# Kernel tuning notes

Measured on AMD Instinct MI355X. Metric: run time of the kernel, lower is better.

## Reference

```python
import jax, jax.numpy as jnp
import numpy as np

B, S, F = 64, 512, 1024
D_MODEL, D_MEM, D_IN, H, D_OUT, N_SYNC, T, H_NLM = 2048, 32, 1024, 16, 1000, 512, 16, 32
DH = D_IN // H


def _ln(x, g, b):
    m = x.mean(-1, keepdims=True)
    v = ((x - m) ** 2).mean(-1, keepdims=True)
    return (x - m) * jax.lax.rsqrt(v + 1e-5) * g + b


def setup_inputs() -> dict:
    key = jax.random.key(0)
    ks = jax.random.split(key, 24)
    def n(i, shape, fan):
        return jax.random.normal(ks[i], shape, jnp.float32) * (fan ** -0.5)
    u = 1.0 / np.sqrt(D_MODEL)
    uh = 1.0 / np.sqrt(D_MODEL + D_MEM)
    return dict(
        x=jax.random.normal(ks[0], (B, S, F), jnp.float32),
        W_kv=n(1, (F, D_IN), F), b_kv=jnp.zeros((D_IN,)),
        g_kv=jnp.ones((D_IN,)), be_kv=jnp.zeros((D_IN,)),
        W_q=n(2, (N_SYNC, D_IN), N_SYNC), b_q=jnp.zeros((D_IN,)),
        W_aq=n(3, (D_IN, D_IN), D_IN), b_aq=jnp.zeros((D_IN,)),
        W_ak=n(4, (D_IN, D_IN), D_IN), b_ak=jnp.zeros((D_IN,)),
        W_av=n(5, (D_IN, D_IN), D_IN), b_av=jnp.zeros((D_IN,)),
        W_ao=n(6, (D_IN, D_IN), D_IN), b_ao=jnp.zeros((D_IN,)),
        W_s1=n(7, (D_IN + D_MODEL, D_MODEL), D_IN + D_MODEL), b_s1=jnp.zeros((D_MODEL,)),
        W_s2=n(8, (D_MODEL, D_MODEL), D_MODEL), b_s2=jnp.zeros((D_MODEL,)),
        g_s=jnp.ones((D_MODEL,)), be_s=jnp.zeros((D_MODEL,)),
        W_n1=n(9, (D_MODEL, D_MEM, H_NLM), D_MEM), b_n1=jnp.zeros((D_MODEL, H_NLM)),
        W_n2=n(10, (D_MODEL, H_NLM), H_NLM), b_n2=jnp.zeros((D_MODEL,)),
        g_n=jnp.ones((D_MODEL,)), be_n=jnp.zeros((D_MODEL,)),
        init_state=jax.random.uniform(ks[11], (D_MODEL,), jnp.float32, -u, u),
        init_hist=jax.random.uniform(ks[12], (D_MODEL, D_MEM), jnp.float32, -uh, uh),
        decay_action=jax.random.uniform(ks[13], (N_SYNC,), jnp.float32, 0.0, 2.0),
        decay_out=jax.random.uniform(ks[14], (N_SYNC,), jnp.float32, 0.0, 2.0),
        W_out=n(15, (N_SYNC, D_OUT), N_SYNC), b_out=jnp.zeros((D_OUT,)),
        idx_la=jax.random.randint(ks[16], (N_SYNC,), 0, D_MODEL),
        idx_ra=jax.random.randint(ks[17], (N_SYNC,), 0, D_MODEL),
        idx_lo=jax.random.randint(ks[18], (N_SYNC,), 0, D_MODEL),
        idx_ro=jax.random.randint(ks[19], (N_SYNC,), 0, D_MODEL),
    )


def reference(x, W_kv, b_kv, g_kv, be_kv, W_q, b_q, W_aq, b_aq, W_ak, b_ak,
              W_av, b_av, W_ao, b_ao, W_s1, b_s1, W_s2, b_s2, g_s, be_s,
              W_n1, b_n1, W_n2, b_n2, g_n, be_n, init_state, init_hist,
              decay_action, decay_out, W_out, b_out,
              idx_la, idx_ra, idx_lo, idx_ro):
    # kv features: Linear + LayerNorm, fixed across ticks -> project k,v once
    kv = _ln(x @ W_kv + b_kv, g_kv, be_kv)                      # (B,S,D_IN)
    kh = (kv @ W_ak + b_ak).reshape(B, S, H, DH)
    vh = (kv @ W_av + b_av).reshape(B, S, H, DH)
    # learnable exponential decay r = exp(-clamp(p,0,15))
    rA = jnp.exp(-jnp.clip(decay_action, 0.0, 15.0))[None, :]
    rO = jnp.exp(-jnp.clip(decay_out, 0.0, 15.0))[None, :]
    act0 = jnp.broadcast_to(init_state, (B, D_MODEL))
    hist0 = jnp.broadcast_to(init_hist, (B, D_MODEL, D_MEM))
    # out-sync initialized before loop (None branch): alpha=prod, beta=1
    aO0 = act0[:, idx_lo] * act0[:, idx_ro]
    bO0 = jnp.ones_like(aO0)
    # action-sync None branch at tick0 == recurrence from alpha=beta=0
    aA0 = jnp.zeros((B, N_SYNC), x.dtype)
    bA0 = jnp.zeros((B, N_SYNC), x.dtype)

    def step(carry, _):
        act, hist, aA, bA, aO, bO = carry
        pA = act[:, idx_la] * act[:, idx_ra]                    # paired-neuron gather
        aA = rA * aA + pA
        bA = rA * bA + 1.0
        sync_a = aA * jax.lax.rsqrt(bA)
        q = sync_a @ W_q + b_q                                  # (B,D_IN)
        qh = (q @ W_aq + b_aq).reshape(B, H, DH)
        attn_w = jax.nn.softmax(jnp.einsum('bhd,bshd->bhs', qh, kh) / np.sqrt(DH), axis=-1)
        attn = jnp.einsum('bhs,bshd->bhd', attn_w, vh).reshape(B, D_IN) @ W_ao + b_ao
        pre = jnp.concatenate([attn, act], axis=-1)             # (B, D_IN+D_MODEL)
        pre_act = _ln(jax.nn.gelu(pre @ W_s1 + b_s1) @ W_s2 + b_s2, g_s, be_s)
        hist = jnp.concatenate([hist[:, :, 1:], pre_act[:, :, None]], axis=-1)
        # per-neuron deep NLM over the memory window
        hmid = jax.nn.relu(jnp.einsum('bdm,dmh->bdh', hist, W_n1) + b_n1)
        act = _ln(jnp.einsum('bdh,dh->bd', hmid, W_n2) + b_n2, g_n, be_n)
        pO = act[:, idx_lo] * act[:, idx_ro]
        aO = rO * aO + pO
        bO = rO * bO + 1.0
        pred = (aO * jax.lax.rsqrt(bO)) @ W_out + b_out         # (B,D_OUT)
        logp = jax.nn.log_softmax(pred, axis=-1)
        ne = -(jnp.exp(logp) * logp).sum(-1) / np.log(D_OUT)    # normalized entropy
        return (act, hist, aA, bA, aO, bO), (pred, ne)

    _, (preds, nes) = jax.lax.scan(step, (act0, hist0, aA0, bA0, aO0, bO0), None, length=T)
    predictions = jnp.transpose(preds, (1, 2, 0))               # (B,D_OUT,T)
    certainties = jnp.transpose(jnp.stack([nes, 1.0 - nes], axis=1), (2, 1, 0))  # (B,2,T)
    return predictions, certainties
```

## Files before the change

kernel.cpp:

```cpp
#include <hip/hip_runtime.h>
#include <hip/hip_bf16.h>


#define B_ 64
#define S_ 512
#define F_ 1024
#define DMODEL 2048
#define DMEM 32
#define DIN 1024
#define NH 16
#define DH 64
#define DOUT 1000
#define NSYNC 512
#define TICKS 16
#define HNLM 32
#define HIST_W 48

typedef __attribute__((ext_vector_type(8))) short short8;
typedef __attribute__((ext_vector_type(4))) float f32x4;

__device__ inline void store_f(float* p, float v) { *p = v; }
__device__ inline void store_f(__hip_bfloat16* p, float v) { *p = __float2bfloat16(v); }

__device__ inline short f2bs(float f) {
  __hip_bfloat16 h = __float2bfloat16(f);
  return *reinterpret_cast<short*>(&h);
}

__device__ inline float bfs(short x) {
  return __uint_as_float(((unsigned)(unsigned short)x) << 16);
}

__device__ inline float gelu_f(float x) {
  float x3 = x * x * x;
  return 0.5f * x * (1.f + tanhf(0.7978845608028654f * (x + 0.044715f * x3)));
}

__device__ inline float bf_lo(unsigned v) { return __uint_as_float(v << 16); }
__device__ inline float bf_hi(unsigned v) { return __uint_as_float(v & 0xffff0000u); }

__global__ __launch_bounds__(256) void transpose_bf16_kernel(const float* __restrict__ W,
                                                             __hip_bfloat16* __restrict__ Wt,
                                                             int K, int N, int Npad, int ldw,
                                                             int koff) {
  __shared__ float t[32][33];
  const int tx = threadIdx.x, ty = threadIdx.y;
  const int n0 = blockIdx.x * 32, k0 = blockIdx.y * 32;
#pragma unroll
  for (int i = 0; i < 4; i++) {
    int k = k0 + ty + i * 8;
    t[ty + i * 8][tx] = (k < K && n0 + tx < N) ? W[(size_t)k * N + n0 + tx] : 0.f;
  }
  __syncthreads();
#pragma unroll
  for (int i = 0; i < 4; i++) {
    int n = n0 + ty + i * 8;
    if (n < Npad && k0 + tx < K)
      Wt[(size_t)n * ldw + koff + k0 + tx] = __float2bfloat16(t[tx][ty + i * 8]);
  }
}

__global__ void conv_bf16_kernel(const float* __restrict__ src, __hip_bfloat16* __restrict__ dst,
                                 int n) {
  int i = blockIdx.x * 256 + threadIdx.x;
  if (i < n) dst[i] = __float2bfloat16(src[i]);
}

__global__ void bqaq_kernel(const float* __restrict__ b_q, const float* __restrict__ b_aq,
                            const __hip_bfloat16* __restrict__ Wt_aq, float* __restrict__ b_qaq) {
  int n = blockIdx.x * 256 + threadIdx.x;
  if (n >= DIN) return;
  const __hip_bfloat16* wr = Wt_aq + (size_t)n * DIN;
  float s = b_aq[n];
  for (int k = 0; k < DIN; k++) s += b_q[k] * __bfloat162float(wr[k]);
  b_qaq[n] = s;
}

__global__ void bs1c_kernel(const float* __restrict__ b_s1, const float* __restrict__ b_ao,
                            const float* __restrict__ W_s1, float* __restrict__ b_s1c) {
  int n = blockIdx.x * 256 + threadIdx.x;
  if (n >= DMODEL) return;
  float s = b_s1[n];
  for (int k = 0; k < DIN; k++) s += b_ao[k] * W_s1[(size_t)k * DMODEL + n];
  b_s1c[n] = s;
}

__device__ inline short8 load_chunk(const __hip_bfloat16* p) {
  return *reinterpret_cast<const short8*>(p);
}
__device__ inline short8 load_chunk(const float* p) {
  short8 r;
#pragma unroll
  for (int j = 0; j < 8; j++) r[j] = f2bs(p[j]);
  return r;
}

template <int TRANSC, typename TA, typename TC>
__global__ __launch_bounds__(256) void gemm_big(const TA* __restrict__ A,
                                                const __hip_bfloat16* __restrict__ Bt,
                                                const float* __restrict__ bias,
                                                TC* __restrict__ C, int M, int N, int K) {
  __shared__ short lsA[128 * 64];
  __shared__ short lsB[128 * 64];
  const int tid = threadIdx.x;
  const int l = tid & 63, w = tid >> 6;
  const int wr = (w >> 1) * 64, wc = (w & 1) * 64;
  const int nwg = gridDim.x * gridDim.y;
  const int flat = blockIdx.y * gridDim.x + blockIdx.x;
  const int wk = (flat & 7) * (nwg >> 3) + (flat >> 3);
  const int brow = (wk / gridDim.x) * 128, bcol = (wk % gridDim.x) * 128;
  f32x4 acc[4][4];
#pragma unroll
  for (int i = 0; i < 4; i++)
#pragma unroll
    for (int j = 0; j < 4; j++)
#pragma unroll
      for (int r = 0; r < 4; r++) acc[i][j][r] = 0.f;

  short8 ra[4], rb[4];
  auto gload = [&](int k0) {
#pragma unroll
    for (int q = 0; q < 4; q++) {
      int i = tid + q * 256;
      int row = i >> 3, c = i & 7;
      ra[q] = load_chunk(A + (size_t)(brow + row) * K + k0 + c * 8);
      rb[q] = load_chunk(Bt + (size_t)(bcol + row) * K + k0 + c * 8);
    }
  };
  auto lwrite = [&]() {
#pragma unroll
    for (int q = 0; q < 4; q++) {
      int i = tid + q * 256;
      int row = i >> 3, c = i & 7;
      int sw = c ^ (row & 7);
      *reinterpret_cast<short8*>(&lsA[row * 64 + sw * 8]) = ra[q];
      *reinterpret_cast<short8*>(&lsB[row * 64 + sw * 8]) = rb[q];
    }
  };
  gload(0);
  for (int k0 = 0; k0 < K; k0 += 64) {
    __syncthreads();
    lwrite();
    if (k0 + 64 < K) gload(k0 + 64);
    __syncthreads();
#pragma unroll
    for (int ks = 0; ks < 2; ks++) {
      short8 af[4], bfv[4];
#pragma unroll
      for (int mi = 0; mi < 4; mi++) {
        int row = wr + mi * 16 + (l & 15);
        int c = ks * 4 + (l >> 4);
        af[mi] = *reinterpret_cast<const short8*>(&lsA[row * 64 + (c ^ (row & 7)) * 8]);
      }
#pragma unroll
      for (int ni = 0; ni < 4; ni++) {
        int row = wc + ni * 16 + (l & 15);
        int c = ks * 4 + (l >> 4);
        bfv[ni] = *reinterpret_cast<const short8*>(&lsB[row * 64 + (c ^ (row & 7)) * 8]);
      }
#pragma unroll
      for (int mi = 0; mi < 4; mi++)
#pragma unroll
        for (int ni = 0; ni < 4; ni++)
          acc[mi][ni] =
              __builtin_amdgcn_mfma_f32_16x16x32_bf16(af[mi], bfv[ni], acc[mi][ni], 0, 0, 0);
    }
  }
#pragma unroll
  for (int mi = 0; mi < 4; mi++)
#pragma unroll
    for (int ni = 0; ni < 4; ni++)
#pragma unroll
      for (int r = 0; r < 4; r++) {
        int row = brow + wr + mi * 16 + (l >> 4) * 4 + r;
        int col = bcol + wc + ni * 16 + (l & 15);
        float v = acc[mi][ni][r];
        if (bias) v += bias[col];
        if (TRANSC == 1) {
          store_f(&C[(size_t)col * M + row], v);
        } else if (TRANSC == 2) {
          int bb = row >> 9, s = row & 511, hh = col >> 6, dd = col & 63;
          store_f(&C[(((size_t)(bb * 16 + hh) * 512) + s) * 64 + dd], v);
        } else if (TRANSC == 3) {
          int bb = row >> 9, s = row & 511, hh2 = col >> 6, dd = col & 63;
          size_t base = (hh2 >= 16) ? (size_t)B_ * S_ * DIN : 0;
          store_f(&C[base + (((size_t)(bb * 16 + (hh2 & 15)) * 512) + s) * 64 + dd], v);
        } else {
          store_f(&C[(size_t)row * N + col], v);
        }
      }
}

template <typename TOUT>
__global__ __launch_bounds__(256) void ln_kernel(const float* __restrict__ x,
                                                 const float* __restrict__ g,
                                                 const float* __restrict__ be,
                                                 TOUT* __restrict__ out, int C,
                                                 size_t row_stride, int col_stride) {
  const int row = blockIdx.x;
  const int tid = threadIdx.x;
  const float* xr = x + (size_t)row * C;
  float s = 0.f, s2 = 0.f;
  for (int c = tid; c < C; c += 256) {
    float v = xr[c];
    s += v;
    s2 += v * v;
  }
  __shared__ float r1[256], r2[256];
  r1[tid] = s;
  r2[tid] = s2;
  __syncthreads();
  for (int st = 128; st > 0; st >>= 1) {
    if (tid < st) {
      r1[tid] += r1[tid + st];
      r2[tid] += r2[tid + st];
    }
    __syncthreads();
  }
  float mean = r1[0] / C;
  float var = r2[0] / C - mean * mean;
  float inv = 1.0f / sqrtf(var + 1e-5f);
  for (int c = tid; c < C; c += 256) {
    float v = (xr[c] - mean) * inv * g[c] + be[c];
    store_f(&out[(size_t)row * row_stride + (size_t)c * col_stride], v);
  }
}

__global__ void init_pre_kernel(const float* __restrict__ init_state,
                                __hip_bfloat16* __restrict__ pre) {
  int i = blockIdx.x * 256 + threadIdx.x;
  if (i >= B_ * DMODEL) return;
  int b = i >> 11, j = i & (DMODEL - 1);
  pre[(size_t)b * 3072 + DIN + j] = __float2bfloat16(init_state[j]);
}

__global__ void init_hist_kernel(const float* __restrict__ init_hist, float* __restrict__ hist) {
  int i = blockIdx.x * 256 + threadIdx.x;
  if (i >= B_ * DMODEL * DMEM) return;
  int m = i & (DMEM - 1);
  int bd = i >> 5;
  int d = bd & (DMODEL - 1);
  hist[(size_t)bd * HIST_W + m] = init_hist[d * DMEM + m];
}

__global__ void init_sync_kernel(const float* __restrict__ init_state,
                                 const float* __restrict__ decay_action,
                                 const float* __restrict__ decay_out,
                                 const int* __restrict__ la, const int* __restrict__ ra,
                                 const int* __restrict__ lo, const int* __restrict__ ro,
                                 float* __restrict__ aA, float* __restrict__ bA,
                                 float* __restrict__ aO, float* __restrict__ bO,
                                 __hip_bfloat16* __restrict__ syncA, float* __restrict__ rAv,
                                 float* __restrict__ rOv) {
  int i = blockIdx.x * 256 + threadIdx.x;
  if (i >= B_ * NSYNC) return;
  int j = i & (NSYNC - 1);
  if (i < NSYNC) {
    rAv[i] = expf(-fminf(fmaxf(decay_action[i], 0.f), 15.f));
    rOv[i] = expf(-fminf(fmaxf(decay_out[i], 0.f), 15.f));
  }
  float pA = init_state[la[j]] * init_state[ra[j]];
  aA[i] = pA;
  bA[i] = 1.f;
  syncA[i] = __float2bfloat16(pA);
  aO[i] = init_state[lo[j]] * init_state[ro[j]];
  bO[i] = 1.f;
}

template <typename EPI>
__device__ __forceinline__ void mm_tile64(const __hip_bfloat16* __restrict__ A, int lda,
                                          const __hip_bfloat16* __restrict__ Bt, int ldb,
                                          int bcol, int kb, int kchunk, int tid, short* lsA,
                                          short* lsB, EPI epi) {
  const int l = tid & 63, w = tid >> 6;
  f32x4 acc[4];
#pragma unroll
  for (int i = 0; i < 4; i++)
#pragma unroll
    for (int r = 0; r < 4; r++) acc[i][r] = 0.f;
  short8 ra[2], rb[2];
  auto gload = [&](int k0) {
#pragma unroll
    for (int q = 0; q < 2; q++) {
      int i = tid + q * 256;
      int row = i >> 3, c = i & 7;
      ra[q] = *reinterpret_cast<const short8*>(A + (size_t)row * lda + k0 + c * 8);
      rb[q] = *reinterpret_cast<const short8*>(Bt + (size_t)(bcol + row) * ldb + k0 + c * 8);
    }
  };
  auto lwrite = [&]() {
#pragma unroll
    for (int q = 0; q < 2; q++) {
      int i = tid + q * 256;
      int row = i >> 3, c = i & 7;
      int sw = c ^ (row & 7);
      *reinterpret_cast<short8*>(&lsA[row * 64 + sw * 8]) = ra[q];
      *reinterpret_cast<short8*>(&lsB[row * 64 + sw * 8]) = rb[q];
    }
  };
  gload(kb);
  for (int k0 = kb; k0 < kb + kchunk; k0 += 64) {
    __syncthreads();
    lwrite();
    if (k0 + 64 < kb + kchunk) gload(k0 + 64);
    __syncthreads();
#pragma unroll
    for (int ks = 0; ks < 2; ks++) {
      int rowa = w * 16 + (l & 15);
      int c = ks * 4 + (l >> 4);
      short8 af = *reinterpret_cast<const short8*>(&lsA[rowa * 64 + (c ^ (rowa & 7)) * 8]);
#pragma unroll
      for (int ni = 0; ni < 4; ni++) {
        int rowb = ni * 16 + (l & 15);
        short8 bfv = *reinterpret_cast<const short8*>(&lsB[rowb * 64 + (c ^ (rowb & 7)) * 8]);
        acc[ni] = __builtin_amdgcn_mfma_f32_16x16x32_bf16(af, bfv, acc[ni], 0, 0, 0);
      }
    }
  }
#pragma unroll
  for (int ni = 0; ni < 4; ni++)
#pragma unroll
    for (int r = 0; r < 4; r++) {
      int m = w * 16 + (l >> 4) * 4 + r;
      int n = bcol + ni * 16 + (l & 15);
      epi(m, n, acc[ni][r]);
    }
}

__global__ __launch_bounds__(256) void gemm_part(const __hip_bfloat16* __restrict__ A, int lda,
                                                 const __hip_bfloat16* __restrict__ Bt, int ldb,
                                                 float* __restrict__ part, int N, int kchunk) {
  __shared__ short lsA[64 * 64];
  __shared__ short lsB[64 * 64];
  const int tid = threadIdx.x;
  const int nt = blockIdx.x, ks = blockIdx.y;
  mm_tile64(A, lda, Bt, ldb, nt * 64, ks * kchunk, kchunk, tid, lsA, lsB,
            [&](int m, int n, float v) { part[((size_t)(ks * 64 + m)) * N + n] = v; });
}

__global__ void s1_red_kernel(const float* __restrict__ part, const float* __restrict__ bias,
                              __hip_bfloat16* __restrict__ h1, int KS) {
  int i = blockIdx.x * 256 + threadIdx.x;
  int m = i >> 11, n = i & 2047;
  float s = bias[n];
  for (int k = 0; k < KS; k++) s += part[((size_t)(k * 64 + m)) * DMODEL + n];
  h1[(size_t)m * DMODEL + n] = __float2bfloat16(gelu_f(s));
}

__global__ __launch_bounds__(256) void s2_red_ln_kernel(const float* __restrict__ part,
                                                        const float* __restrict__ bias,
                                                        const float* __restrict__ g,
                                                        const float* __restrict__ be,
                                                        float* __restrict__ hist, int KS, int t) {
  __shared__ float r1[256], r2[256];
  const int b = blockIdx.x;
  const int tid = threadIdx.x;
  float v8[8];
  float s = 0.f, s2 = 0.f;
#pragma unroll
  for (int i = 0; i < 8; i++) {
    int n = tid + i * 256;
    float x = bias[n];
    for (int k = 0; k < KS; k++) x += part[((size_t)(k * 64 + b)) * DMODEL + n];
    v8[i] = x;
    s += x;
    s2 += x * x;
  }
  r1[tid] = s;
  r2[tid] = s2;
  __syncthreads();
  for (int st = 128; st > 0; st >>= 1) {
    if (tid < st) {
      r1[tid] += r1[tid + st];
      r2[tid] += r2[tid + st];
    }
    __syncthreads();
  }
  float mean = r1[0] / DMODEL;
  float var = r2[0] / DMODEL - mean * mean;
  float inv = 1.f / sqrtf(var + 1e-5f);
#pragma unroll
  for (int i = 0; i < 8; i++) {
    int n = tid + i * 256;
    float pa = (v8[i] - mean) * inv * g[n] + be[n];
    hist[((size_t)b * DMODEL + n) * HIST_W + 32 + t] = pa;
  }
}

__global__ __launch_bounds__(256) void attn_kernel(const float* __restrict__ qpart,
                                                   const float* __restrict__ b_qaq,
                                                   const __hip_bfloat16* __restrict__ kh,
                                                   const __hip_bfloat16* __restrict__ vh,
                                                   __hip_bfloat16* __restrict__ pre) {
  __shared__ float qs[64];
  __shared__ float wv[512];
  __shared__ float red[256];
  __shared__ float red2[2048];
  const int u = blockIdx.x;
  const int b = u >> 4, h = u & (NH - 1);
  const int tid = threadIdx.x;
  const __hip_bfloat16* Kp = kh + (size_t)u * (S_ * DH);
  const __hip_bfloat16* Vp = vh + (size_t)u * (S_ * DH);
  if (tid < DH) {
    int n = h * DH + tid;
    float s = b_qaq[n];
#pragma unroll
    for (int ks = 0; ks < 4; ks++) s += qpart[((size_t)(ks * 64 + b)) * DIN + n];
    qs[tid] = s;
  }
  __syncthreads();
  float sc[2];
#pragma unroll
  for (int r = 0; r < 2; ++r) {
    int s = tid + r * 256;
    const short8* kp = reinterpret_cast<const short8*>(Kp + (size_t)s * DH);
    float accv = 0.f;
#pragma unroll
    for (int q = 0; q < 8; ++q) {
      short8 kk = kp[q];
#pragma unroll
      for (int j = 0; j < 8; ++j) accv += qs[q * 8 + j] * bfs(kk[j]);
    }
    sc[r] = accv * 0.125f;
  }
  red[tid] = fmaxf(sc[0], sc[1]);
  __syncthreads();
  for (int st = 128; st > 0; st >>= 1) {
    if (tid < st) red[tid] = fmaxf(red[tid], red[tid + st]);
    __syncthreads();
  }
  const float mx = red[0];
  __syncthreads();
  float e0 = expf(sc[0] - mx), e1 = expf(sc[1] - mx);
  wv[tid] = e0;
  wv[tid + 256] = e1;
  red[tid] = e0 + e1;
  __syncthreads();
  for (int st = 128; st > 0; st >>= 1) {
    if (tid < st) red[tid] += red[tid + st];
    __syncthreads();
  }
  const float invZ = 1.f / red[0];
  __syncthreads();
  const int d8 = tid & 7, sg = tid >> 3;
  float pacc[8];
#pragma unroll
  for (int j = 0; j < 8; ++j) pacc[j] = 0.f;
  for (int s = sg; s < S_; s += 32) {
    float wgt = wv[s];
    short8 vvv = *reinterpret_cast<const short8*>(Vp + (size_t)s * DH + d8 * 8);
#pragma unroll
    for (int j = 0; j < 8; ++j) pacc[j] += wgt * bfs(vvv[j]);
  }
#pragma unroll
  for (int j = 0; j < 8; ++j) red2[sg * 64 + d8 * 8 + j] = pacc[j];
  __syncthreads();
  if (tid < DH) {
    float r = 0.f;
#pragma unroll
    for (int g2 = 0; g2 < 32; ++g2) r += red2[g2 * 64 + tid];
    pre[(size_t)b * 3072 + h * DH + tid] = __float2bfloat16(r * invZ);
  }
}

__global__ __launch_bounds__(256) void nlm_kernel(const float* __restrict__ hist,
                                                  const float* __restrict__ W1,
                                                  const float* __restrict__ b1,
                                                  const float* __restrict__ W2,
                                                  const float* __restrict__ b2,
                                                  float* __restrict__ out, int t) {
  __shared__ float w1s[4096];
  __shared__ float b1s[128];
  const int tid = threadIdx.x;
  const int d0 = blockIdx.x * 4;
  for (int i = tid; i < 4096; i += 256) w1s[i] = W1[(size_t)d0 * 1024 + i];
  if (tid < 128) b1s[tid] = b1[d0 * 32 + tid];
  __syncthreads();
  const int b = tid & 63, dsub = tid >> 6;
  const int d = d0 + dsub;
  const float* hw = hist + ((size_t)(b * DMODEL + d)) * HIST_W + (t + 1);
  float win[DMEM];
#pragma unroll
  for (int m = 0; m < DMEM; ++m) win[m] = hw[m];
  const float* w1 = w1s + dsub * 1024;
  const float* bb = b1s + dsub * 32;
  const float* w2 = W2 + d * HNLM;
  float acc = 0.f;
  for (int h = 0; h < HNLM; ++h) {
    float s = bb[h];
#pragma unroll
    for (int m = 0; m < DMEM; ++m) s += win[m] * w1[m * HNLM + h];
    acc += fmaxf(s, 0.f) * w2[h];
  }
  out[(size_t)b * DMODEL + d] = acc + b2[d];
}

__global__ __launch_bounds__(256) void final_kernel(
    const float* __restrict__ nlmraw, const float* __restrict__ g_n,
    const float* __restrict__ be_n, const int* __restrict__ la, const int* __restrict__ ra,
    const int* __restrict__ lo, const int* __restrict__ ro, const float* __restrict__ rAv,
    const float* __restrict__ rOv, float* __restrict__ aA, float* __restrict__ bA,
    float* __restrict__ aO, float* __restrict__ bO, __hip_bfloat16* __restrict__ syncA,
    __hip_bfloat16* __restrict__ pre, const __hip_bfloat16* __restrict__ Wt_out,
    const float* __restrict__ b_out, float* __restrict__ outp, int t) {
  __shared__ float arow[2048];
  __shared__ float so_p[520];
  __shared__ float pv[1024];
  __shared__ float red[256], red2[256];
  const int b = blockIdx.x;
  const int tid = threadIdx.x;
  const float* xr = nlmraw + (size_t)b * DMODEL;
  float xv[8];
  float s = 0.f, s2 = 0.f;
#pragma unroll
  for (int i = 0; i < 8; i++) {
    float x = xr[tid + i * 256];
    xv[i] = x;
    s += x;
    s2 += x * x;
  }
  red[tid] = s;
  red2[tid] = s2;
  __syncthreads();
  for (int st = 128; st > 0; st >>= 1) {
    if (tid < st) {
      red[tid] += red[tid + st];
      red2[tid] += red2[tid + st];
    }
    __syncthreads();
  }
  float mean = red[0] / DMODEL;
  float var = red2[0] / DMODEL - mean * mean;
  float inv = 1.f / sqrtf(var + 1e-5f);
  __syncthreads();
#pragma unroll
  for (int i = 0; i < 8; i++) {
    int n = tid + i * 256;
    float av = (xv[i] - mean) * inv * g_n[n] + be_n[n];
    arow[n] = av;
    pre[(size_t)b * 3072 + DIN + n] = __float2bfloat16(av);
  }
  __syncthreads();
  for (int j = tid; j < NSYNC; j += 256) {
    size_t idx = (size_t)b * NSYNC + j;
    float pA = arow[la[j]] * arow[ra[j]];
    float r = rAv[j];
    float av2 = r * aA[idx] + pA, bv2 = r * bA[idx] + 1.f;
    aA[idx] = av2;
    bA[idx] = bv2;
    syncA[idx] = __float2bfloat16(av2 / sqrtf(bv2));
    float pO = arow[lo[j]] * arow[ro[j]];
    float ro2 = rOv[j];
    float av3 = ro2 * aO[idx] + pO, bv3 = ro2 * bO[idx] + 1.f;
    aO[idx] = av3;
    bO[idx] = bv3;
    so_p[j + (j >> 6)] = av3 / sqrtf(bv3);
  }
  __syncthreads();
  const int lk = tid & 7;
  const int rg = tid >> 3;
  for (int it = 0; it < 32; ++it) {
    int n = it * 32 + rg;
    float sacc = 0.f;
    if (n < DOUT) {
      const short8* wr8 = reinterpret_cast<const short8*>(Wt_out + (size_t)n * NSYNC);
#pragma unroll
      for (int q = 0; q < 8; ++q) {
        short8 w8 = wr8[q * 8 + lk];
#pragma unroll
        for (int j = 0; j < 8; ++j) sacc += so_p[q * 65 + lk * 8 + j] * bfs(w8[j]);
      }
    }
    sacc += __shfl_xor(sacc, 1);
    sacc += __shfl_xor(sacc, 2);
    sacc += __shfl_xor(sacc, 4);
    if (lk == 0 && n < DOUT) pv[n] = sacc + b_out[n];
  }
  __syncthreads();
  float m = -1e30f;
  for (int o = tid; o < DOUT; o += 256) m = fmaxf(m, pv[o]);
  red[tid] = m;
  __syncthreads();
  for (int st = 128; st > 0; st >>= 1) {
    if (tid < st) red[tid] = fmaxf(red[tid], red[tid + st]);
    __syncthreads();
  }
  m = red[0];
  __syncthreads();
  float z = 0.f, s1 = 0.f;
  for (int o = tid; o < DOUT; o += 256) {
    float wv2 = pv[o] - m;
    float e = expf(wv2);
    z += e;
    s1 += e * wv2;
  }
  red[tid] = z;
  __syncthreads();
  for (int st = 128; st > 0; st >>= 1) {
    if (tid < st) red[tid] += red[tid + st];
    __syncthreads();
  }
  const float Z = red[0];
  __syncthreads();
  red[tid] = s1;
  __syncthreads();
  for (int st = 128; st > 0; st >>= 1) {
    if (tid < st) red[tid] += red[tid + st];
    __syncthreads();
  }
  const float S1 = red[0];
  const float ne = -(S1 / Z - logf(Z)) / 6.907755278982137f;
  for (int o = tid; o < DOUT; o += 256) outp[((size_t)b * DOUT + o) * TICKS + t] = pv[o];
  if (tid == 0) {
    float* c = outp + (size_t)B_ * DOUT * TICKS;
    c[b * 2 * TICKS + t] = ne;
    c[b * 2 * TICKS + TICKS + t] = 1.f - ne;
  }
}

extern "C" void kernel_launch(void* const* d_in, const int* in_sizes, int n_in,
                              void* d_out, int out_size, void* d_ws, size_t ws_size,
                              hipStream_t stream) {
  const float* x = (const float*)d_in[0];
  const float* W_kv = (const float*)d_in[1];
  const float* b_kv = (const float*)d_in[2];
  const float* g_kv = (const float*)d_in[3];
  const float* be_kv = (const float*)d_in[4];
  const float* W_q = (const float*)d_in[5];
  const float* b_q = (const float*)d_in[6];
  const float* W_aq = (const float*)d_in[7];
  const float* b_aq = (const float*)d_in[8];
  const float* W_ak = (const float*)d_in[9];
  const float* b_ak = (const float*)d_in[10];
  const float* W_av = (const float*)d_in[11];
  const float* b_av = (const float*)d_in[12];
  const float* W_ao = (const float*)d_in[13];
  const float* b_ao = (const float*)d_in[14];
  const float* W_s1 = (const float*)d_in[15];
  const float* b_s1 = (const float*)d_in[16];
  const float* W_s2 = (const float*)d_in[17];
  const float* b_s2 = (const float*)d_in[18];
  const float* g_s = (const float*)d_in[19];
  const float* be_s = (const float*)d_in[20];
  const float* W_n1 = (const float*)d_in[21];
  const float* b_n1 = (const float*)d_in[22];
  const float* W_n2 = (const float*)d_in[23];
  const float* b_n2 = (const float*)d_in[24];
  const float* g_n = (const float*)d_in[25];
  const float* be_n = (const float*)d_in[26];
  const float* init_state = (const float*)d_in[27];
  const float* init_hist = (const float*)d_in[28];
  const float* decay_action = (const float*)d_in[29];
  const float* decay_out = (const float*)d_in[30];
  const float* W_out = (const float*)d_in[31];
  const float* b_out = (const float*)d_in[32];
  const int* idx_la = (const int*)d_in[33];
  const int* idx_ra = (const int*)d_in[34];
  const int* idx_lo = (const int*)d_in[35];
  const int* idx_ro = (const int*)d_in[36];
  float* out = (float*)d_out;

  char* wsb = (char*)d_ws;
  size_t off = 0;
  auto alloc = [&](size_t bytes) -> char* {
    char* p = wsb + off;
    off += (bytes + 255) & ~(size_t)255;
    return p;
  };
  const size_t MS = (size_t)B_ * S_;
  char* regionA = alloc(MS * DIN * 4);
  __hip_bfloat16* kv = (__hip_bfloat16*)alloc(MS * DIN * 2);
  float* histf = (float*)alloc((size_t)B_ * DMODEL * HIST_W * 4);
  __hip_bfloat16* Wt_kv = (__hip_bfloat16*)alloc((size_t)DIN * F_ * 2);
  __hip_bfloat16* Wt_akav = (__hip_bfloat16*)alloc((size_t)2 * DIN * DIN * 2);
  __hip_bfloat16* Wt_aq = (__hip_bfloat16*)alloc((size_t)DIN * DIN * 2);
  __hip_bfloat16* W_ao_b = (__hip_bfloat16*)alloc((size_t)DIN * DIN * 2);
  __hip_bfloat16* W_qb = (__hip_bfloat16*)alloc((size_t)NSYNC * DIN * 2);
  __hip_bfloat16* Wt_qaq = (__hip_bfloat16*)alloc((size_t)DIN * NSYNC * 2);
  __hip_bfloat16* Wts1top = (__hip_bfloat16*)alloc((size_t)DMODEL * DIN * 2);
  __hip_bfloat16* Wt_s1c = (__hip_bfloat16*)alloc((size_t)DMODEL * (DIN + DMODEL) * 2);
  __hip_bfloat16* Wt_s2 = (__hip_bfloat16*)alloc((size_t)DMODEL * DMODEL * 2);
  __hip_bfloat16* Wt_out = (__hip_bfloat16*)alloc((size_t)DOUT * NSYNC * 2);
  float* b_qaq = (float*)alloc(DIN * 4);
  float* b_s1c = (float*)alloc(DMODEL * 4);
  float* b_akav = (float*)alloc((size_t)2 * DIN * 4);
  float* partial = (float*)alloc((size_t)8 * 64 * DMODEL * 4);
  float* aA = (float*)alloc((size_t)B_ * NSYNC * 4);
  float* bA = (float*)alloc((size_t)B_ * NSYNC * 4);
  float* aO = (float*)alloc((size_t)B_ * NSYNC * 4);
  float* bO = (float*)alloc((size_t)B_ * NSYNC * 4);
  __hip_bfloat16* syncA = (__hip_bfloat16*)alloc((size_t)B_ * NSYNC * 2);
  __hip_bfloat16* pre = (__hip_bfloat16*)alloc((size_t)B_ * (DIN + DMODEL) * 2);
  __hip_bfloat16* h1 = (__hip_bfloat16*)alloc((size_t)B_ * DMODEL * 2);
  float* nlmraw = (float*)alloc((size_t)B_ * DMODEL * 4);
  float* rAv = (float*)alloc(NSYNC * 4);
  float* rOv = (float*)alloc(NSYNC * 4);

  float* kvraw = (float*)regionA;
  __hip_bfloat16* kh = (__hip_bfloat16*)regionA;
  __hip_bfloat16* vh = (__hip_bfloat16*)(regionA + MS * DIN * 2);
  __hip_bfloat16* Wt_ak = Wt_akav;
  __hip_bfloat16* Wt_av = Wt_akav + (size_t)DIN * DIN;

  dim3 t32x8(32, 8);
  transpose_bf16_kernel<<<dim3(F_ / 32, DIN / 32), t32x8, 0, stream>>>(W_kv, Wt_kv, F_, DIN, DIN,
                                                                       F_, 0);
  transpose_bf16_kernel<<<dim3(DIN / 32, DIN / 32), t32x8, 0, stream>>>(W_ak, Wt_ak, DIN, DIN,
                                                                        DIN, DIN, 0);
  transpose_bf16_kernel<<<dim3(DIN / 32, DIN / 32), t32x8, 0, stream>>>(W_av, Wt_av, DIN, DIN,
                                                                        DIN, DIN, 0);
  transpose_bf16_kernel<<<dim3(DIN / 32, DIN / 32), t32x8, 0, stream>>>(W_aq, Wt_aq, DIN, DIN,
                                                                        DIN, DIN, 0);
  transpose_bf16_kernel<<<dim3(DMODEL / 32, DIN / 32), t32x8, 0, stream>>>(W_s1, Wts1top, DIN,
                                                                           DMODEL, DMODEL, DIN, 0);
  transpose_bf16_kernel<<<dim3(DMODEL / 32, DMODEL / 32), t32x8, 0, stream>>>(
      W_s1 + (size_t)DIN * DMODEL, Wt_s1c, DMODEL, DMODEL, DMODEL, DIN + DMODEL, DIN);
  transpose_bf16_kernel<<<dim3(DMODEL / 32, DMODEL / 32), t32x8, 0, stream>>>(W_s2, Wt_s2, DMODEL,
                                                                              DMODEL, DMODEL,
                                                                              DMODEL, 0);
  transpose_bf16_kernel<<<dim3((DOUT + 31) / 32, NSYNC / 32), t32x8, 0, stream>>>(
      W_out, Wt_out, NSYNC, DOUT, DOUT, NSYNC, 0);
  conv_bf16_kernel<<<(NSYNC * DIN + 255) / 256, 256, 0, stream>>>(W_q, W_qb, NSYNC * DIN);
  conv_bf16_kernel<<<(DIN * DIN + 255) / 256, 256, 0, stream>>>(W_ao, W_ao_b, DIN * DIN);
  bqaq_kernel<<<4, 256, 0, stream>>>(b_q, b_aq, Wt_aq, b_qaq);
  bs1c_kernel<<<8, 256, 0, stream>>>(b_s1, b_ao, W_s1, b_s1c);
  hipMemcpyAsync(b_akav, b_ak, DIN * 4, hipMemcpyDeviceToDevice, stream);
  hipMemcpyAsync(b_akav + DIN, b_av, DIN * 4, hipMemcpyDeviceToDevice, stream);

  gemm_big<0, float, float><<<dim3(DIN / 128, MS / 128), 256, 0, stream>>>(x, Wt_kv, b_kv, kvraw,
                                                                           (int)MS, DIN, F_);
  ln_kernel<__hip_bfloat16><<<(int)MS, 256, 0, stream>>>(kvraw, g_kv, be_kv, kv, DIN, DIN, 1);
  gemm_big<3, __hip_bfloat16, __hip_bfloat16><<<dim3(2 * DIN / 128, MS / 128), 256, 0, stream>>>(
      kv, Wt_akav, b_akav, kh, (int)MS, 2 * DIN, DIN);
  gemm_big<1, __hip_bfloat16, __hip_bfloat16><<<dim3(DIN / 128, NSYNC / 128), 256, 0, stream>>>(
      W_qb, Wt_aq, nullptr, Wt_qaq, NSYNC, DIN, DIN);
  gemm_big<1, __hip_bfloat16, __hip_bfloat16><<<dim3(DMODEL / 128, DIN / 128), 256, 0, stream>>>(
      W_ao_b, Wts1top, nullptr, Wt_s1c, DIN + DMODEL, DMODEL, DIN);

  init_pre_kernel<<<(B_ * DMODEL + 255) / 256, 256, 0, stream>>>(init_state, pre);
  init_hist_kernel<<<(B_ * DMODEL * DMEM + 255) / 256, 256, 0, stream>>>(init_hist, histf);
  init_sync_kernel<<<(B_ * NSYNC + 255) / 256, 256, 0, stream>>>(
      init_state, decay_action, decay_out, idx_la, idx_ra, idx_lo, idx_ro, aA, bA, aO, bO, syncA,
      rAv, rOv);

  for (int t = 0; t < TICKS; ++t) {
    gemm_part<<<dim3(16, 4), 256, 0, stream>>>(syncA, NSYNC, Wt_qaq, NSYNC, partial, DIN, 128);
    attn_kernel<<<B_ * NH, 256, 0, stream>>>(partial, b_qaq, kh, vh, pre);
    gemm_part<<<dim3(32, 8), 256, 0, stream>>>(pre, DIN + DMODEL, Wt_s1c, DIN + DMODEL, partial,
                                               DMODEL, 384);
    s1_red_kernel<<<512, 256, 0, stream>>>(partial, b_s1c, h1, 8);
    gemm_part<<<dim3(32, 8), 256, 0, stream>>>(h1, DMODEL, Wt_s2, DMODEL, partial, DMODEL, 256);
    s2_red_ln_kernel<<<B_, 256, 0, stream>>>(partial, b_s2, g_s, be_s, histf, 8, t);
    nlm_kernel<<<DMODEL / 4, 256, 0, stream>>>(histf, W_n1, b_n1, W_n2, b_n2, nlmraw, t);
    final_kernel<<<B_, 256, 0, stream>>>(nlmraw, g_n, be_n, idx_la, idx_ra, idx_lo, idx_ro, rAv,
                                         rOv, aA, bA, aO, bO, syncA, pre, Wt_out, b_out, out, t);
  }
  (void)in_sizes; (void)n_in; (void)out_size; (void)ws_size;
}
```

Measured before the change: 2.615 ms.

## Fuse per-tick query projection into final kernel, dropping gemm_part launch

Moves the sync-to-query projection (syncA @ Wt_qaq + bias) out of a separate split-K gemm_part launch and into the tail of final_kernel. It is computed per batch row from fp32 sync values kept in shared memory, and a new qh0_kernel produces the initial query before the loop. attn_kernel now reads the finished query instead of summing four partials. This removes one launch per tick and the partial-sum round trip through global memory. The cost is that final_kernel, with only 64 blocks, now does an extra 1024x512 dot product per row, which lengthens that kernel.

```diff
diff --git a/kernel.cpp b/kernel.cpp
--- a/kernel.cpp
+++ b/kernel.cpp
@@ -250,7 +250,7 @@
                                  const int* __restrict__ lo, const int* __restrict__ ro,
                                  float* __restrict__ aA, float* __restrict__ bA,
                                  float* __restrict__ aO, float* __restrict__ bO,
-                                 __hip_bfloat16* __restrict__ syncA, float* __restrict__ rAv,
+                                 float* __restrict__ syncA0, float* __restrict__ rAv,
                                  float* __restrict__ rOv) {
   int i = blockIdx.x * 256 + threadIdx.x;
   if (i >= B_ * NSYNC) return;
@@ -262,9 +262,37 @@
   float pA = init_state[la[j]] * init_state[ra[j]];
   aA[i] = pA;
   bA[i] = 1.f;
-  syncA[i] = __float2bfloat16(pA);
+  syncA0[i] = pA;
   aO[i] = init_state[lo[j]] * init_state[ro[j]];
   bO[i] = 1.f;
+}
+
+__global__ __launch_bounds__(256) void qh0_kernel(const float* __restrict__ syncA0,
+                                                  const __hip_bfloat16* __restrict__ Wt_qaq,
+                                                  const float* __restrict__ b_qaq,
+                                                  float* __restrict__ qhb) {
+  __shared__ float sa_p[520];
+  const int b = blockIdx.x;
+  const int tid = threadIdx.x;
+  for (int j = tid; j < NSYNC; j += 256) sa_p[j + (j >> 6)] = syncA0[(size_t)b * NSYNC + j];
+  __syncthreads();
+  const int lk = tid & 7;
+  const int rg = tid >> 3;
+  for (int it = 0; it < 32; ++it) {
+    int n = it * 32 + rg;
+    const short8* wr8 = reinterpret_cast<const short8*>(Wt_qaq + (size_t)n * NSYNC);
+    float sacc = 0.f;
+#pragma unroll
+    for (int q = 0; q < 8; ++q) {
+      short8 w8 = wr8[q * 8 + lk];
+#pragma unroll
+      for (int j = 0; j < 8; ++j) sacc += sa_p[q * 65 + lk * 8 + j] * bfs(w8[j]);
+    }
+    sacc += __shfl_xor(sacc, 1);
+    sacc += __shfl_xor(sacc, 2);
+    sacc += __shfl_xor(sacc, 4);
+    if (lk == 0) qhb[(size_t)b * DIN + n] = sacc + b_qaq[n];
+  }
 }
 
 template <typename EPI>
@@ -387,8 +415,7 @@
   }
 }
 
-__global__ __launch_bounds__(256) void attn_kernel(const float* __restrict__ qpart,
-                                                   const float* __restrict__ b_qaq,
+__global__ __launch_bounds__(256) void attn_kernel(const float* __restrict__ qhb,
                                                    const __hip_bfloat16* __restrict__ kh,
                                                    const __hip_bfloat16* __restrict__ vh,
                                                    __hip_bfloat16* __restrict__ pre) {
@@ -401,13 +428,7 @@
   const int tid = threadIdx.x;
   const __hip_bfloat16* Kp = kh + (size_t)u * (S_ * DH);
   const __hip_bfloat16* Vp = vh + (size_t)u * (S_ * DH);
-  if (tid < DH) {
-    int n = h * DH + tid;
-    float s = b_qaq[n];
-#pragma unroll
-    for (int ks = 0; ks < 4; ks++) s += qpart[((size_t)(ks * 64 + b)) * DIN + n];
-    qs[tid] = s;
-  }
+  if (tid < DH) qs[tid] = qhb[(size_t)b * DIN + h * DH + tid];
   __syncthreads();
   float sc[2];
 #pragma unroll
@@ -500,10 +521,12 @@
     const float* __restrict__ be_n, const int* __restrict__ la, const int* __restrict__ ra,
     const int* __restrict__ lo, const int* __restrict__ ro, const float* __restrict__ rAv,
     const float* __restrict__ rOv, float* __restrict__ aA, float* __restrict__ bA,
-    float* __restrict__ aO, float* __restrict__ bO, __hip_bfloat16* __restrict__ syncA,
-    __hip_bfloat16* __restrict__ pre, const __hip_bfloat16* __restrict__ Wt_out,
+    float* __restrict__ aO, float* __restrict__ bO, __hip_bfloat16* __restrict__ pre,
+    const __hip_bfloat16* __restrict__ Wt_qaq, const float* __restrict__ b_qaq,
+    float* __restrict__ qhb, const __hip_bfloat16* __restrict__ Wt_out,
     const float* __restrict__ b_out, float* __restrict__ outp, int t) {
   __shared__ float arow[2048];
+  __shared__ float sa_p[520];
   __shared__ float so_p[520];
   __shared__ float pv[1024];
   __shared__ float red[256], red2[256];
@@ -548,7 +571,7 @@
     float av2 = r * aA[idx] + pA, bv2 = r * bA[idx] + 1.f;
     aA[idx] = av2;
     bA[idx] = bv2;
-    syncA[idx] = __float2bfloat16(av2 / sqrtf(bv2));
+    sa_p[j + (j >> 6)] = av2 / sqrtf(bv2);
     float pO = arow[lo[j]] * arow[ro[j]];
     float ro2 = rOv[j];
     float av3 = ro2 * aO[idx] + pO, bv3 = ro2 * bO[idx] + 1.f;
@@ -559,6 +582,21 @@
   __syncthreads();
   const int lk = tid & 7;
   const int rg = tid >> 3;
+  for (int it = 0; it < 32; ++it) {
+    int n = it * 32 + rg;
+    const short8* wr8 = reinterpret_cast<const short8*>(Wt_qaq + (size_t)n * NSYNC);
+    float sacc = 0.f;
+#pragma unroll
+    for (int q = 0; q < 8; ++q) {
+      short8 w8 = wr8[q * 8 + lk];
+#pragma unroll
+      for (int j = 0; j < 8; ++j) sacc += sa_p[q * 65 + lk * 8 + j] * bfs(w8[j]);
+    }
+    sacc += __shfl_xor(sacc, 1);
+    sacc += __shfl_xor(sacc, 2);
+    sacc += __shfl_xor(sacc, 4);
+    if (lk == 0) qhb[(size_t)b * DIN + n] = sacc + b_qaq[n];
+  }
   for (int it = 0; it < 32; ++it) {
     int n = it * 32 + rg;
     float sacc = 0.f;
@@ -689,7 +727,8 @@
   float* bA = (float*)alloc((size_t)B_ * NSYNC * 4);
   float* aO = (float*)alloc((size_t)B_ * NSYNC * 4);
   float* bO = (float*)alloc((size_t)B_ * NSYNC * 4);
-  __hip_bfloat16* syncA = (__hip_bfloat16*)alloc((size_t)B_ * NSYNC * 2);
+  float* syncA0 = (float*)alloc((size_t)B_ * NSYNC * 4);
+  float* qhb = (float*)alloc((size_t)B_ * DIN * 4);
   __hip_bfloat16* pre = (__hip_bfloat16*)alloc((size_t)B_ * (DIN + DMODEL) * 2);
   __hip_bfloat16* h1 = (__hip_bfloat16*)alloc((size_t)B_ * DMODEL * 2);
   float* nlmraw = (float*)alloc((size_t)B_ * DMODEL * 4);
@@ -740,12 +779,12 @@
   init_pre_kernel<<<(B_ * DMODEL + 255) / 256, 256, 0, stream>>>(init_state, pre);
   init_hist_kernel<<<(B_ * DMODEL * DMEM + 255) / 256, 256, 0, stream>>>(init_hist, histf);
   init_sync_kernel<<<(B_ * NSYNC + 255) / 256, 256, 0, stream>>>(
-      init_state, decay_action, decay_out, idx_la, idx_ra, idx_lo, idx_ro, aA, bA, aO, bO, syncA,
-      rAv, rOv);
+      init_state, decay_action, decay_out, idx_la, idx_ra, idx_lo, idx_ro, aA, bA, aO, bO,
+      syncA0, rAv, rOv);
+  qh0_kernel<<<B_, 256, 0, stream>>>(syncA0, Wt_qaq, b_qaq, qhb);
 
   for (int t = 0; t < TICKS; ++t) {
-    gemm_part<<<dim3(16, 4), 256, 0, stream>>>(syncA, NSYNC, Wt_qaq, NSYNC, partial, DIN, 128);
-    attn_kernel<<<B_ * NH, 256, 0, stream>>>(partial, b_qaq, kh, vh, pre);
+    attn_kernel<<<B_ * NH, 256, 0, stream>>>(qhb, kh, vh, pre);
     gemm_part<<<dim3(32, 8), 256, 0, stream>>>(pre, DIN + DMODEL, Wt_s1c, DIN + DMODEL, partial,
                                                DMODEL, 384);
     s1_red_kernel<<<512, 256, 0, stream>>>(partial, b_s1c, h1, 8);
@@ -753,7 +792,8 @@
     s2_red_ln_kernel<<<B_, 256, 0, stream>>>(partial, b_s2, g_s, be_s, histf, 8, t);
     nlm_kernel<<<DMODEL / 4, 256, 0, stream>>>(histf, W_n1, b_n1, W_n2, b_n2, nlmraw, t);
     final_kernel<<<B_, 256, 0, stream>>>(nlmraw, g_n, be_n, idx_la, idx_ra, idx_lo, idx_ro, rAv,
-                                         rOv, aA, bA, aO, bO, syncA, pre, Wt_out, b_out, out, t);
+                                         rOv, aA, bA, aO, bO, pre, Wt_qaq, b_qaq, qhb, Wt_out,
+                                         b_out, out, t);
   }
   (void)in_sizes; (void)n_in; (void)out_size; (void)ws_size;
 }
```

Result: slower. 4.049 ms (+54.8%).
